# Kernel optimization log

Hardware: AMD Instinct MI355X
Metric: run time of the kernel (lower is better)

## Reference

```python
import jax, jax.numpy as jnp
import numpy as np
import math

B, T, N, E = 16, 12, 2000, 8000
D, GAT_HEADS, NHEAD, FF, L, HORIZON = 64, 4, 4, 128, 2, 3
M = B * N  # batched node count


def setup_inputs() -> dict:
    key = jax.random.key(0)
    ks = jax.random.split(key, 16)

    def nrm(k, shape, s=0.1):
        return jax.random.normal(k, shape, jnp.float32) * s

    return dict(
        x_seq=jax.random.normal(ks[0], (B, T, N), jnp.float32),
        edge_index=jax.random.randint(ks[1], (2, E), 0, N),
        # GATConv 1: in_dim=1 -> 4 heads x 8 = 32
        W1=nrm(ks[2], (1, 32)),
        att_src1=nrm(ks[3], (GAT_HEADS, 8)),
        att_dst1=nrm(ks[4], (GAT_HEADS, 8)),
        b1=jnp.zeros((32,), jnp.float32),
        # GATConv 2: 32 -> 4 heads x 16 = 64
        W2=nrm(ks[5], (32, 64)),
        att_src2=nrm(ks[6], (GAT_HEADS, 16)),
        att_dst2=nrm(ks[7], (GAT_HEADS, 16)),
        b2=jnp.zeros((64,), jnp.float32),
        # TransformerEncoder (post-LN, relu), stacked over L layers
        Wqkv=nrm(ks[8], (L, 3 * D, D)), bqkv=jnp.zeros((L, 3 * D), jnp.float32),
        Wo=nrm(ks[9], (L, D, D)), bo=jnp.zeros((L, D), jnp.float32),
        Wf1=nrm(ks[10], (L, FF, D)), bf1=jnp.zeros((L, FF), jnp.float32),
        Wf2=nrm(ks[11], (L, D, FF)), bf2=jnp.zeros((L, D), jnp.float32),
        g1=jnp.ones((L, D), jnp.float32), be1=jnp.zeros((L, D), jnp.float32),
        g2=jnp.ones((L, D), jnp.float32), be2=jnp.zeros((L, D), jnp.float32),
        # prediction head
        Wh=nrm(ks[12], (HORIZON, D)), bh=jnp.zeros((HORIZON,), jnp.float32),
    )


def _layer_norm(x, g, b, eps=1e-5):
    mu = x.mean(-1, keepdims=True)
    var = ((x - mu) ** 2).mean(-1, keepdims=True)
    return (x - mu) * jax.lax.rsqrt(var + eps) * g + b


def _gat(x, src, dst, W, a_src, a_dst, bias, H, C, num_nodes):
    # PyG GATConv (concat=True, eval mode). x: [M, in] -> [M, H*C]
    h = (x @ W).reshape(-1, H, C)                                  # [M,H,C]
    e = jax.nn.leaky_relu((h * a_src).sum(-1)[src] + (h * a_dst).sum(-1)[dst], 0.2)  # [Etot,H]
    m = jax.ops.segment_max(e, dst, num_segments=num_nodes)
    w = jnp.exp(e - m[dst])
    s = jax.ops.segment_sum(w, dst, num_segments=num_nodes)
    alpha = w / (s[dst] + 1e-16)
    out = jax.ops.segment_sum(h[src] * alpha[:, :, None], dst, num_segments=num_nodes)
    return out.reshape(-1, H * C) + bias


def _forward(x_seq, edge_index, W1, att_src1, att_dst1, b1, W2, att_src2, att_dst2, b2,
             Wqkv, bqkv, Wo, bo, Wf1, bf1, Wf2, bf2, g1, be1, g2, be2, Wh, bh):
    # batch edge index with per-graph node offsets, then add self loops (PyG default)
    offs = (jnp.arange(B) * N)[:, None]
    loops = jnp.arange(M)
    src = jnp.concatenate([(edge_index[0][None] + offs).reshape(-1), loops])
    dst = jnp.concatenate([(edge_index[1][None] + offs).reshape(-1), loops])

    xt = x_seq.transpose(1, 0, 2).reshape(T, M, 1)  # per-timestep node features

    def gnn_step(x):
        h = jax.nn.relu(_gat(x, src, dst, W1, att_src1, att_dst1, b1, GAT_HEADS, 8, M))
        return jax.nn.relu(_gat(h, src, dst, W2, att_src2, att_dst2, b2, GAT_HEADS, 16, M))

    seq = jax.vmap(gnn_step)(xt)  # [T, M, D]

    # sinusoidal positional encoding over time axis
    pos = jnp.arange(T, dtype=jnp.float32)[:, None]
    div = jnp.exp(jnp.arange(0, D, 2, dtype=jnp.float32) * (-math.log(10000.0) / D))
    pe = jnp.zeros((T, D), jnp.float32)
    pe = pe.at[:, 0::2].set(jnp.sin(pos * div)).at[:, 1::2].set(jnp.cos(pos * div))
    seq = seq + pe[:, None, :]

    hd = D // NHEAD
    scale = 1.0 / math.sqrt(hd)
    for i in range(L):  # post-LN transformer encoder layers
        qkv = seq @ Wqkv[i].T + bqkv[i]
        q, k, v = jnp.split(qkv, 3, axis=-1)
        q = q.reshape(T, M, NHEAD, hd)
        k = k.reshape(T, M, NHEAD, hd)
        v = v.reshape(T, M, NHEAD, hd)
        sc = jnp.einsum('tmhd,smhd->mhts', q, k) * scale  # [M,H,T,T]
        attn = jax.nn.softmax(sc, axis=-1)
        o = jnp.einsum('mhts,smhd->tmhd', attn, v).reshape(T, M, D)
        seq = _layer_norm(seq + (o @ Wo[i].T + bo[i]), g1[i], be1[i])
        ff = jax.nn.relu(seq @ Wf1[i].T + bf1[i]) @ Wf2[i].T + bf2[i]
        seq = _layer_norm(seq + ff, g2[i], be2[i])

    final = seq[-1]  # [M, D]
    return (final @ Wh.T + bh).reshape(B, N, HORIZON).transpose(0, 2, 1)  # [B, horizon, N]


def reference(x_seq, edge_index, W1, att_src1, att_dst1, b1, W2, att_src2, att_dst2, b2,
              Wqkv, bqkv, Wo, bo, Wf1, bf1, Wf2, bf2, g1, be1, g2, be2, Wh, bh):
    return _forward(x_seq, edge_index, W1, att_src1, att_dst1, b1, W2, att_src2, att_dst2, b2,
                    Wqkv, bqkv, Wo, bo, Wf1, bf1, Wf2, bf2, g1, be1, g2, be2, Wh, bh)
```

## Files before the change

### kernel.cpp

```cpp
#include <hip/hip_runtime.h>
#include <hip/hip_bf16.h>

#define B_ 16
#define T_ 12
#define N_ 2000
#define E_ 8000
#define M_ 32000
#define ETOT (B_*E_ + M_)
#define D_ 64

typedef __hip_bfloat16 bf16;
typedef unsigned short u16;
typedef __attribute__((ext_vector_type(8))) _Float16 half8;
typedef __attribute__((ext_vector_type(2))) _Float16 h2v;
typedef __attribute__((ext_vector_type(4))) float f32x4;

__device__ __forceinline__ float bfu(u16 u){ return __uint_as_float(((unsigned int)u)<<16); }
__device__ __forceinline__ u16 f2bu(float f){
  unsigned int x = __float_as_uint(f);
  x += 0x7FFFu + ((x >> 16) & 1u);
  return (u16)(x >> 16);
}
__device__ __forceinline__ u16 f2h(float f){
  _Float16 h = (_Float16)f; u16 r; __builtin_memcpy(&r, &h, 2); return r;
}
__device__ __forceinline__ float h2f(u16 u){
  _Float16 h; __builtin_memcpy(&h, &u, 2); return (float)h;
}
__device__ __forceinline__ h2v u2h(unsigned u){ h2v r; __builtin_memcpy(&r,&u,4); return r; }

__global__ void k_prep(const float* __restrict__ Wqkv, const float* __restrict__ Wo,
                       const float* __restrict__ Wf1, const float* __restrict__ Wf2,
                       u16* __restrict__ wqB, u16* __restrict__ woB,
                       u16* __restrict__ w1B, u16* __restrict__ w2B,
                       float* __restrict__ peT){
  int i = blockIdx.x*256 + threadIdx.x;
  if(i < 24576){
    int l=i/12288, r=i-l*12288;
    int nt=r>>10, r2=r&1023, c=r2>>9, r3=r2&511, lane=r3>>3, jj=r3&7;
    int m=lane&15, q=lane>>4;
    wqB[i] = f2h(Wqkv[l*12288 + (nt*16+m)*64 + c*32 + q*8 + jj]);
  } else if(i < 32768){
    int k2=i-24576;
    int l=k2>>12, r=k2&4095;
    int nt=r>>10, r2=r&1023, c=r2>>9, r3=r2&511, lane=r3>>3, jj=r3&7;
    int m=lane&15, q=lane>>4;
    woB[k2] = f2h(Wo[l*4096 + (nt*16+m)*64 + c*32 + q*8 + jj]);
  } else if(i < 49152){
    int k2=i-32768;
    int l=k2>>13, r=k2&8191;
    int nt=r>>10, r2=r&1023, c=r2>>9, r3=r2&511, lane=r3>>3, jj=r3&7;
    int m=lane&15, q=lane>>4;
    w1B[k2] = f2h(Wf1[l*8192 + (nt*16+m)*64 + c*32 + q*8 + jj]);
  } else if(i < 65536){
    int k2=i-49152;
    int l=k2>>13, r=k2&8191;
    int nt=r>>11, r2=r&2047, c=r2>>9, r3=r2&511, lane=r3>>3, jj=r3&7;
    int m=lane&15, q=lane>>4;
    w2B[k2] = f2h(Wf2[l*8192 + (nt*16+m)*128 + c*32 + q*8 + jj]);
  } else {
    int i2 = i - 65536;
    if(i2 < 768){
      int t=i2>>6, ch=i2&63;
      float ang = (float)t * __expf(-0.14391156463f * (float)(ch & ~1));
      peT[i2] = (ch&1) ? __cosf(ang) : __sinf(ang);
    }
  }
}

__global__ void k_zero(int* __restrict__ p, int n){
  int i = blockIdx.x*256 + threadIdx.x; if(i<n) p[i]=0;
}

__global__ void k_hist(const int* __restrict__ ei, int* __restrict__ deg){
  int e = blockIdx.x*256 + threadIdx.x; if(e>=ETOT) return;
  int dst;
  if (e < B_*E_){ int b = e / E_; int k = e - b*E_; dst = ei[E_ + k] + b*N_; }
  else dst = e - B_*E_;
  atomicAdd(&deg[dst], 1);
}

__global__ void k_scan1(const int* __restrict__ deg, int* __restrict__ offs, int* __restrict__ bsums){
  __shared__ int s[256];
  int tid = threadIdx.x; int g = blockIdx.x*256 + tid;
  s[tid] = deg[g]; __syncthreads();
  for(int off=1; off<256; off<<=1){
    int a = (tid>=off) ? s[tid-off] : 0; __syncthreads();
    s[tid] += a; __syncthreads();
  }
  offs[g+1] = s[tid];
  if(tid==255) bsums[blockIdx.x] = s[255];
}

__global__ void k_scan2(const int* __restrict__ bsums, int* __restrict__ boffs){
  __shared__ int s[128];
  int tid = threadIdx.x;
  int v = (tid<125) ? bsums[tid] : 0;
  s[tid] = v; __syncthreads();
  for(int off=1; off<128; off<<=1){
    int a = (tid>=off) ? s[tid-off] : 0; __syncthreads();
    s[tid] += a; __syncthreads();
  }
  if(tid<125) boffs[tid] = s[tid] - v;
}

__global__ void k_scan3(int* __restrict__ offs, const int* __restrict__ boffs){
  int tid = threadIdx.x; int g = blockIdx.x*256 + tid;
  offs[g+1] += boffs[blockIdx.x];
  if(g==0) offs[0]=0;
}

__global__ void k_scatter(const int* __restrict__ ei, const int* __restrict__ offs,
                          int* __restrict__ cursor, int* __restrict__ csr){
  int e = blockIdx.x*256 + threadIdx.x; if(e>=ETOT) return;
  int src, dst;
  if (e < B_*E_){ int b=e/E_; int k=e-b*E_; src=ei[k]+b*N_; dst=ei[E_+k]+b*N_; }
  else { src = e - B_*E_; dst = src; }
  int pos = atomicAdd(&cursor[dst], 1);
  csr[offs[dst]+pos] = src;
}

__global__ __launch_bounds__(256) void k_gat12(
  const float* __restrict__ x_seq, const float* __restrict__ W1,
  const float* __restrict__ as1, const float* __restrict__ ad1, const float* __restrict__ b1,
  const float* __restrict__ W2, const float* __restrict__ as2, const float* __restrict__ ad2,
  const int* __restrict__ offs, const int* __restrict__ csr,
  u16* __restrict__ h2u, float* __restrict__ asc, float* __restrict__ adc)
{
  __shared__ float W2s[2048];
  __shared__ float a2s[64], a2d[64];
  int tid = threadIdx.x;
  for(int i=tid;i<2048;i+=256) W2s[i]=W2[i];
  if(tid<64){ a2s[tid]=as2[tid]; a2d[tid]=ad2[tid]; }
  __syncthreads();

  int t = blockIdx.y;
  int id = blockIdx.x*256 + tid;
  int m = id>>2, l4 = id&3;

  float sS[4], sD[4];
  #pragma unroll
  for(int h=0;h<4;h++){
    float a=0.f, d=0.f;
    #pragma unroll
    for(int c=0;c<8;c++){ float w=W1[h*8+c]; a+=w*as1[h*8+c]; d+=w*ad1[h*8+c]; }
    sS[h]=a; sD[h]=d;
  }
  unsigned um=(unsigned)m, b=um/N_, n=um-b*N_;
  const float* xsl = x_seq + (size_t)(b*T_+t)*N_;
  float xm = xsl[n];
  int e0=offs[m], e1=offs[m+1];
  float sum[4]={0,0,0,0}, ax[4]={0,0,0,0};
  for(int e=e0+l4; e<e1; e+=4){
    unsigned s=(unsigned)csr[e]; unsigned sn=s - (s/N_)*N_;
    float xv = xsl[sn];
    #pragma unroll
    for(int h=0;h<4;h++){
      float ee = xv*sS[h] + xm*sD[h]; ee = ee>0.f ? ee : 0.2f*ee;
      float w = __expf(ee); sum[h]+=w; ax[h]+=w*xv;
    }
  }
  float A[4];
  #pragma unroll
  for(int h=0;h<4;h++){
    sum[h] += __shfl_xor(sum[h],1); sum[h] += __shfl_xor(sum[h],2);
    ax[h]  += __shfl_xor(ax[h],1);  ax[h]  += __shfl_xor(ax[h],2);
    A[h] = ax[h]/(sum[h]+1e-16f);
  }

  float acc[16];
  #pragma unroll
  for(int c=0;c<16;c++) acc[c]=0.f;
  #pragma unroll
  for(int k=0;k<32;k++){
    int hs = k>>3;
    float v = A[hs]*W1[k] + b1[k]; v = v>0.f ? v : 0.f;
    #pragma unroll
    for(int c=0;c<16;c++) acc[c] += v*W2s[k*64 + l4*16 + c];
  }
  uint2* hp = (uint2*)(h2u + ((size_t)t*M_ + m)*64 + l4*16);
  #pragma unroll
  for(int c2=0;c2<4;c2++){
    uint2 p;
    p.x = (unsigned)f2bu(acc[4*c2+0]) | ((unsigned)f2bu(acc[4*c2+1])<<16);
    p.y = (unsigned)f2bu(acc[4*c2+2]) | ((unsigned)f2bu(acc[4*c2+3])<<16);
    hp[c2] = p;
  }
  float ss=0.f, sd=0.f;
  #pragma unroll
  for(int c=0;c<16;c++){ ss += acc[c]*a2s[l4*16+c]; sd += acc[c]*a2d[l4*16+c]; }
  asc[((size_t)t*M_+m)*4+l4]=ss; adc[((size_t)t*M_+m)*4+l4]=sd;
}

__global__ __launch_bounds__(256) void k_gat2b(
  const u16* __restrict__ h2u, const float* __restrict__ asc, const float* __restrict__ adc,
  const float* __restrict__ b2, const int* __restrict__ offs, const int* __restrict__ csr,
  const float* __restrict__ peT, u16* __restrict__ seq)
{
  int t = blockIdx.y;
  int id = blockIdx.x*256 + threadIdx.x;
  int m = id>>2, h = id&3;
  float am = adc[((size_t)t*M_+m)*4+h];
  int e0=offs[m], e1=offs[m+1];
  float sum=0.f;
  float A[16];
  #pragma unroll
  for(int c=0;c<16;c++) A[c]=0.f;
  for(int e=e0;e<e1;e++){
    int s=csr[e];
    float ee = asc[((size_t)t*M_+s)*4+h] + am; ee = ee>0.f ? ee : 0.2f*ee;
    float w = __expf(ee); sum += w;
    const uint2* hp = (const uint2*)(h2u + ((size_t)t*M_ + s)*64 + h*16);
    #pragma unroll
    for(int c2=0;c2<4;c2++){
      uint2 p = hp[c2];
      A[4*c2+0] += w*bfu((u16)(p.x));
      A[4*c2+1] += w*bfu((u16)(p.x>>16));
      A[4*c2+2] += w*bfu((u16)(p.y));
      A[4*c2+3] += w*bfu((u16)(p.y>>16));
    }
  }
  float inv = 1.f/(sum + 1e-16f);
  #pragma unroll
  for(int c=0;c<16;c++){
    int ch = h*16 + c;
    float v = A[c]*inv + b2[ch]; v = v>0.f ? v : 0.f;
    seq[((size_t)t*M_ + m)*64 + ch] = f2h(v + peT[t*64+ch]);
  }
}

__global__ __launch_bounds__(192) void k_layer2(
  u16* __restrict__ seq,
  const u16* __restrict__ wqB, const u16* __restrict__ woB,
  const u16* __restrict__ w1B, const u16* __restrict__ w2B,
  const float* __restrict__ bqkv, const float* __restrict__ bo,
  const float* __restrict__ bf1,  const float* __restrict__ bf2,
  const float* __restrict__ g1,   const float* __restrict__ be1,
  const float* __restrict__ g2,   const float* __restrict__ be2)
{
  __shared__ __align__(16) u16 X[3456];
  __shared__ __align__(16) u16 QKV[10368];
  u16* Hd = QKV + 3456;
  int tid=threadIdx.x, w=tid>>6, lane=tid&63;
  int m=lane&15, q=lane>>4;
  int r = w*16 + m;

  int trr[4]; size_t base_rr[4];
  #pragma unroll
  for(int rg=0;rg<4;rg++){
    int rc = w*16 + q*4 + rg;
    int nn = rc/12; trr[rg] = rc - nn*12;
    base_rr[rg] = ((size_t)trr[rg]*M_ + (size_t)blockIdx.x*4 + nn)*64;
  }

  #pragma unroll
  for(int rr=0; rr<16; rr++){
    int row = w*16+rr;
    int nn = row/12, tt = row-nn*12;
    X[row*72+lane] = seq[((size_t)tt*M_ + (size_t)blockIdx.x*4+nn)*64 + lane];
  }

  #pragma unroll 1
  for(int l=0; l<2; l++){
    const half8* wqv = (const half8*)(wqB + l*24576/2*0 + (size_t)l*12288);
    const half8* wov = (const half8*)(woB + (size_t)l*4096);
    const half8* w1v = (const half8*)(w1B + (size_t)l*8192);
    const half8* w2v = (const half8*)(w2B + (size_t)l*8192);
    const float* bq = bqkv + l*192;
    const float* boL = bo + l*64;
    const float* b1L = bf1 + l*128;
    const float* b2L = bf2 + l*64;
    const float* g1L = g1 + l*64, *be1L = be1 + l*64;
    const float* g2L = g2 + l*64, *be2L = be2 + l*64;

    half8 xa0 = *(const half8*)&X[r*72 + q*8];
    half8 xa1 = *(const half8*)&X[r*72 + 32 + q*8];
    #pragma unroll
    for(int nt=0; nt<12; nt++){
      f32x4 acc={0.f,0.f,0.f,0.f};
      acc = __builtin_amdgcn_mfma_f32_16x16x32_f16(xa0, wqv[(nt*2+0)*64+lane], acc,0,0,0);
      acc = __builtin_amdgcn_mfma_f32_16x16x32_f16(xa1, wqv[(nt*2+1)*64+lane], acc,0,0,0);
      int cg = nt*16+m; float bias = bq[cg];
      int s = nt>>2, lc = cg&63;
      #pragma unroll
      for(int rg=0;rg<4;rg++){
        int row = w*16 + q*4 + rg;
        QKV[s*3456 + row*72 + lc] = f2h(acc[rg]+bias);
      }
    }
    __syncthreads();

    {
      int an = tid/48, rem = tid - an*48;
      int ah = rem/12, at = rem - ah*12;
      u16* qrow = &QKV[(an*12+at)*72 + ah*16];
      uint4 qa = ((const uint4*)qrow)[0], qb = ((const uint4*)qrow)[1];
      float s[12];
      #pragma unroll
      for(int t2=0;t2<12;t2++){
        const uint4* kp = (const uint4*)&QKV[3456 + (an*12+t2)*72 + ah*16];
        uint4 ka=kp[0], kb=kp[1];
        float d=0.f;
        d=__builtin_amdgcn_fdot2(u2h(qa.x),u2h(ka.x),d,false);
        d=__builtin_amdgcn_fdot2(u2h(qa.y),u2h(ka.y),d,false);
        d=__builtin_amdgcn_fdot2(u2h(qa.z),u2h(ka.z),d,false);
        d=__builtin_amdgcn_fdot2(u2h(qa.w),u2h(ka.w),d,false);
        d=__builtin_amdgcn_fdot2(u2h(qb.x),u2h(kb.x),d,false);
        d=__builtin_amdgcn_fdot2(u2h(qb.y),u2h(kb.y),d,false);
        d=__builtin_amdgcn_fdot2(u2h(qb.z),u2h(kb.z),d,false);
        d=__builtin_amdgcn_fdot2(u2h(qb.w),u2h(kb.w),d,false);
        s[t2] = d*0.25f;
      }
      float mx=s[0];
      #pragma unroll
      for(int t2=1;t2<12;t2++) mx=fmaxf(mx,s[t2]);
      float sum=0.f;
      #pragma unroll
      for(int t2=0;t2<12;t2++){ s[t2]=__expf(s[t2]-mx); sum+=s[t2]; }
      float inv=1.f/sum;
      half8 o0, o1;
      #pragma unroll
      for(int i=0;i<8;i++){ o0[i]=(_Float16)0.f; o1[i]=(_Float16)0.f; }
      #pragma unroll
      for(int t2=0;t2<12;t2++){
        const half8* vr = (const half8*)&QKV[6912 + (an*12+t2)*72 + ah*16];
        _Float16 wh = (_Float16)s[t2];
        o0 += vr[0]*wh; o1 += vr[1]*wh;
      }
      _Float16 ih = (_Float16)inv;
      ((half8*)qrow)[0]=o0*ih; ((half8*)qrow)[1]=o1*ih;
    }
    __syncthreads();

    half8 oa0 = *(const half8*)&QKV[r*72 + q*8];
    half8 oa1 = *(const half8*)&QKV[r*72 + 32 + q*8];
    float y[4][4];
    #pragma unroll
    for(int nt=0;nt<4;nt++){
      f32x4 acc={0.f,0.f,0.f,0.f};
      acc = __builtin_amdgcn_mfma_f32_16x16x32_f16(oa0, wov[(nt*2+0)*64+lane], acc,0,0,0);
      acc = __builtin_amdgcn_mfma_f32_16x16x32_f16(oa1, wov[(nt*2+1)*64+lane], acc,0,0,0);
      int col=nt*16+m; float bias=boL[col];
      #pragma unroll
      for(int rg=0;rg<4;rg++)
        y[nt][rg] = acc[rg] + bias + h2f(X[(w*16+q*4+rg)*72 + col]);
    }
    float mu[4], rs[4];
    #pragma unroll
    for(int rg=0;rg<4;rg++){
      float sm=(y[0][rg]+y[1][rg])+(y[2][rg]+y[3][rg]);
      sm+=__shfl_xor(sm,1); sm+=__shfl_xor(sm,2); sm+=__shfl_xor(sm,4); sm+=__shfl_xor(sm,8);
      mu[rg]=sm*(1.f/64.f);
      float d0=y[0][rg]-mu[rg],d1=y[1][rg]-mu[rg],d2=y[2][rg]-mu[rg],d3=y[3][rg]-mu[rg];
      float vv=(d0*d0+d1*d1)+(d2*d2+d3*d3);
      vv+=__shfl_xor(vv,1); vv+=__shfl_xor(vv,2); vv+=__shfl_xor(vv,4); vv+=__shfl_xor(vv,8);
      rs[rg]=rsqrtf(vv*(1.f/64.f)+1e-5f);
    }
    #pragma unroll
    for(int nt=0;nt<4;nt++){
      int col=nt*16+m; float g=g1L[col], be=be1L[col];
      #pragma unroll
      for(int rg=0;rg<4;rg++){
        float v=(y[nt][rg]-mu[rg])*rs[rg]*g+be;
        y[nt][rg]=v;
        QKV[(w*16+q*4+rg)*72 + col]=f2h(v);
      }
    }

    half8 ya0 = *(const half8*)&QKV[r*72 + q*8];
    half8 ya1 = *(const half8*)&QKV[r*72 + 32 + q*8];
    #pragma unroll
    for(int nt=0;nt<8;nt++){
      f32x4 acc={0.f,0.f,0.f,0.f};
      acc = __builtin_amdgcn_mfma_f32_16x16x32_f16(ya0, w1v[(nt*2+0)*64+lane], acc,0,0,0);
      acc = __builtin_amdgcn_mfma_f32_16x16x32_f16(ya1, w1v[(nt*2+1)*64+lane], acc,0,0,0);
      float bias=b1L[nt*16+m];
      #pragma unroll
      for(int rg=0;rg<4;rg++)
        Hd[(w*16+q*4+rg)*136 + nt*16+m] = f2h(fmaxf(acc[rg]+bias, 0.f));
    }

    half8 ha[4];
    #pragma unroll
    for(int c=0;c<4;c++)
      ha[c] = *(const half8*)&Hd[r*136 + c*32 + q*8];
    #pragma unroll
    for(int nt=0;nt<4;nt++){
      f32x4 acc={0.f,0.f,0.f,0.f};
      #pragma unroll
      for(int c=0;c<4;c++)
        acc = __builtin_amdgcn_mfma_f32_16x16x32_f16(ha[c], w2v[(nt*4+c)*64+lane], acc,0,0,0);
      int col=nt*16+m; float bias=b2L[col];
      #pragma unroll
      for(int rg=0;rg<4;rg++)
        y[nt][rg] = acc[rg] + bias + y[nt][rg];
    }
    #pragma unroll
    for(int rg=0;rg<4;rg++){
      float sm=(y[0][rg]+y[1][rg])+(y[2][rg]+y[3][rg]);
      sm+=__shfl_xor(sm,1); sm+=__shfl_xor(sm,2); sm+=__shfl_xor(sm,4); sm+=__shfl_xor(sm,8);
      mu[rg]=sm*(1.f/64.f);
      float d0=y[0][rg]-mu[rg],d1=y[1][rg]-mu[rg],d2=y[2][rg]-mu[rg],d3=y[3][rg]-mu[rg];
      float vv=(d0*d0+d1*d1)+(d2*d2+d3*d3);
      vv+=__shfl_xor(vv,1); vv+=__shfl_xor(vv,2); vv+=__shfl_xor(vv,4); vv+=__shfl_xor(vv,8);
      rs[rg]=rsqrtf(vv*(1.f/64.f)+1e-5f);
    }
    if(l==0){
      #pragma unroll
      for(int nt=0;nt<4;nt++){
        int col=nt*16+m; float g=g2L[col], be=be2L[col];
        #pragma unroll
        for(int rg=0;rg<4;rg++)
          X[(w*16+q*4+rg)*72 + col] = f2h((y[nt][rg]-mu[rg])*rs[rg]*g + be);
      }
      __syncthreads();
    } else {
      #pragma unroll
      for(int nt=0;nt<4;nt++){
        int col=nt*16+m; float g=g2L[col], be=be2L[col];
        #pragma unroll
        for(int rg=0;rg<4;rg++){
          if(trr[rg]==11)
            seq[base_rr[rg] + col] = f2h((y[nt][rg]-mu[rg])*rs[rg]*g + be);
        }
      }
    }
  }
}

__global__ void k_head(const u16* __restrict__ seq, const float* __restrict__ Wh,
                       const float* __restrict__ bh, float* __restrict__ out){
  int m = blockIdx.x*256 + threadIdx.x; if(m>=M_) return;
  const u16* row = seq + ((size_t)11*M_ + m)*64;
  float a0=bh[0], a1=bh[1], a2=bh[2];
  #pragma unroll
  for(int d=0;d<64;d++){
    float x = h2f(row[d]);
    a0 += x*Wh[d]; a1 += x*Wh[64+d]; a2 += x*Wh[128+d];
  }
  unsigned b=(unsigned)m/N_, n=(unsigned)m-b*N_;
  out[(b*3+0)*N_+n] = a0;
  out[(b*3+1)*N_+n] = a1;
  out[(b*3+2)*N_+n] = a2;
}

extern "C" void kernel_launch(void* const* d_in, const int* in_sizes, int n_in,
                              void* d_out, int out_size, void* d_ws, size_t ws_size,
                              hipStream_t stream)
{
  const float* x_seq=(const float*)d_in[0];
  const int*   ei   =(const int*)d_in[1];
  const float* W1   =(const float*)d_in[2];
  const float* as1  =(const float*)d_in[3];
  const float* ad1  =(const float*)d_in[4];
  const float* b1   =(const float*)d_in[5];
  const float* W2   =(const float*)d_in[6];
  const float* as2  =(const float*)d_in[7];
  const float* ad2  =(const float*)d_in[8];
  const float* b2   =(const float*)d_in[9];
  const float* Wqkv =(const float*)d_in[10];
  const float* bqkv =(const float*)d_in[11];
  const float* Wo   =(const float*)d_in[12];
  const float* bo   =(const float*)d_in[13];
  const float* Wf1  =(const float*)d_in[14];
  const float* bf1p =(const float*)d_in[15];
  const float* Wf2  =(const float*)d_in[16];
  const float* bf2p =(const float*)d_in[17];
  const float* g1   =(const float*)d_in[18];
  const float* be1  =(const float*)d_in[19];
  const float* g2   =(const float*)d_in[20];
  const float* be2  =(const float*)d_in[21];
  const float* Wh   =(const float*)d_in[22];
  const float* bh   =(const float*)d_in[23];

  u16* seqh   = (u16*)d_ws;
  float* asc  = (float*)(seqh + 24576000);
  float* adc  = asc + 1536000;
  int* deg    = (int*)(adc + 1536000);
  int* cursor = deg + M_;
  int* offs   = cursor + M_;
  int* bsums  = offs + (M_ + 2);
  int* boffs  = bsums + 128;
  int* csr    = boffs + 128;
  u16* h2u    = (u16*)(csr + ETOT);
  u16* wqB    = h2u + (size_t)T_*M_*64;
  u16* woB    = wqB + 24576;
  u16* w1B    = woB + 8192;
  u16* w2B    = w1B + 16384;
  float* peT  = (float*)(w2B + 16384);

  k_prep   <<<dim3(260), dim3(256), 0, stream>>>(Wqkv, Wo, Wf1, Wf2, wqB, woB, w1B, w2B, peT);

  k_zero   <<<dim3((2*M_+255)/256), dim3(256), 0, stream>>>(deg, 2*M_);
  k_hist   <<<dim3((ETOT+255)/256), dim3(256), 0, stream>>>(ei, deg);
  k_scan1  <<<dim3(125), dim3(256), 0, stream>>>(deg, offs, bsums);
  k_scan2  <<<dim3(1),   dim3(128), 0, stream>>>(bsums, boffs);
  k_scan3  <<<dim3(125), dim3(256), 0, stream>>>(offs, boffs);
  k_scatter<<<dim3((ETOT+255)/256), dim3(256), 0, stream>>>(ei, offs, cursor, csr);

  k_gat12<<<dim3(500,T_), dim3(256), 0, stream>>>(x_seq, W1, as1, ad1, b1,
                                                  W2, as2, ad2, offs, csr, h2u, asc, adc);
  k_gat2b<<<dim3(500,T_), dim3(256), 0, stream>>>(h2u, asc, adc, b2, offs, csr, peT, seqh);

  k_layer2<<<dim3(8000), dim3(192), 0, stream>>>(seqh,
      wqB, woB, w1B, w2B,
      bqkv, bo, bf1p, bf2p,
      g1, be1, g2, be2);

  k_head<<<dim3(125), dim3(256), 0, stream>>>(seqh, Wh, bh, (float*)d_out);
}
```

Before: 415.0 us.

## Transpose MFMA operands in transformer layer, vectorize LDS stores, store local CSR indices

```diff
diff --git a/kernel.cpp b/kernel.cpp
--- a/kernel.cpp
+++ b/kernel.cpp
@@ -28,6 +28,9 @@
   _Float16 h; __builtin_memcpy(&h, &u, 2); return (float)h;
 }
 __device__ __forceinline__ h2v u2h(unsigned u){ h2v r; __builtin_memcpy(&r,&u,4); return r; }
+__device__ __forceinline__ unsigned pk2(float a, float b){
+  return (unsigned)f2h(a) | ((unsigned)f2h(b)<<16);
+}
 
 __global__ void k_prep(const float* __restrict__ Wqkv, const float* __restrict__ Wo,
                        const float* __restrict__ Wf1, const float* __restrict__ Wf2,
@@ -68,10 +71,6 @@
   }
 }
 
-__global__ void k_zero(int* __restrict__ p, int n){
-  int i = blockIdx.x*256 + threadIdx.x; if(i<n) p[i]=0;
-}
-
 __global__ void k_hist(const int* __restrict__ ei, int* __restrict__ deg){
   int e = blockIdx.x*256 + threadIdx.x; if(e>=ETOT) return;
   int dst;
@@ -113,11 +112,11 @@
 __global__ void k_scatter(const int* __restrict__ ei, const int* __restrict__ offs,
                           int* __restrict__ cursor, int* __restrict__ csr){
   int e = blockIdx.x*256 + threadIdx.x; if(e>=ETOT) return;
-  int src, dst;
-  if (e < B_*E_){ int b=e/E_; int k=e-b*E_; src=ei[k]+b*N_; dst=ei[E_+k]+b*N_; }
-  else { src = e - B_*E_; dst = src; }
+  int srcl, dst;
+  if (e < B_*E_){ int b=e/E_; int k=e-b*E_; srcl=ei[k]; dst=ei[E_+k]+b*N_; }
+  else { dst = e - B_*E_; int b=dst/N_; srcl = dst - b*N_; }
   int pos = atomicAdd(&cursor[dst], 1);
-  csr[offs[dst]+pos] = src;
+  csr[offs[dst]+pos] = srcl;
 }
 
 __global__ __launch_bounds__(256) void k_gat12(
@@ -152,8 +151,7 @@
   int e0=offs[m], e1=offs[m+1];
   float sum[4]={0,0,0,0}, ax[4]={0,0,0,0};
   for(int e=e0+l4; e<e1; e+=4){
-    unsigned s=(unsigned)csr[e]; unsigned sn=s - (s/N_)*N_;
-    float xv = xsl[sn];
+    float xv = xsl[csr[e]];
     #pragma unroll
     for(int h=0;h<4;h++){
       float ee = xv*sS[h] + xm*sD[h]; ee = ee>0.f ? ee : 0.2f*ee;
@@ -200,6 +198,8 @@
   int t = blockIdx.y;
   int id = blockIdx.x*256 + threadIdx.x;
   int m = id>>2, h = id&3;
+  unsigned um=(unsigned)m, b=um/N_;
+  size_t base_s = (size_t)t*M_ + (size_t)b*N_;
   float am = adc[((size_t)t*M_+m)*4+h];
   int e0=offs[m], e1=offs[m+1];
   float sum=0.f;
@@ -207,10 +207,10 @@
   #pragma unroll
   for(int c=0;c<16;c++) A[c]=0.f;
   for(int e=e0;e<e1;e++){
-    int s=csr[e];
-    float ee = asc[((size_t)t*M_+s)*4+h] + am; ee = ee>0.f ? ee : 0.2f*ee;
+    size_t s = base_s + (unsigned)csr[e];
+    float ee = asc[s*4+h] + am; ee = ee>0.f ? ee : 0.2f*ee;
     float w = __expf(ee); sum += w;
-    const uint2* hp = (const uint2*)(h2u + ((size_t)t*M_ + s)*64 + h*16);
+    const uint2* hp = (const uint2*)(h2u + s*64 + h*16);
     #pragma unroll
     for(int c2=0;c2<4;c2++){
       uint2 p = hp[c2];
@@ -244,14 +244,9 @@
   int tid=threadIdx.x, w=tid>>6, lane=tid&63;
   int m=lane&15, q=lane>>4;
   int r = w*16 + m;
-
-  int trr[4]; size_t base_rr[4];
-  #pragma unroll
-  for(int rg=0;rg<4;rg++){
-    int rc = w*16 + q*4 + rg;
-    int nn = rc/12; trr[rg] = rc - nn*12;
-    base_rr[rg] = ((size_t)trr[rg]*M_ + (size_t)blockIdx.x*4 + nn)*64;
-  }
+  int nr = r/12, tr = r - nr*12;
+  int node_r = blockIdx.x*4 + nr;
+  size_t xoff = ((size_t)tr*M_ + node_r)*64;
 
   #pragma unroll
   for(int rr=0; rr<16; rr++){
@@ -262,7 +257,7 @@
 
   #pragma unroll 1
   for(int l=0; l<2; l++){
-    const half8* wqv = (const half8*)(wqB + l*24576/2*0 + (size_t)l*12288);
+    const half8* wqv = (const half8*)(wqB + (size_t)l*12288);
     const half8* wov = (const half8*)(woB + (size_t)l*4096);
     const half8* w1v = (const half8*)(w1B + (size_t)l*8192);
     const half8* w2v = (const half8*)(w2B + (size_t)l*8192);
@@ -273,20 +268,20 @@
     const float* g1L = g1 + l*64, *be1L = be1 + l*64;
     const float* g2L = g2 + l*64, *be2L = be2 + l*64;
 
-    half8 xa0 = *(const half8*)&X[r*72 + q*8];
-    half8 xa1 = *(const half8*)&X[r*72 + 32 + q*8];
+    half8 xb0 = *(const half8*)&X[r*72 + q*8];
+    half8 xb1 = *(const half8*)&X[r*72 + 32 + q*8];
     #pragma unroll
     for(int nt=0; nt<12; nt++){
       f32x4 acc={0.f,0.f,0.f,0.f};
-      acc = __builtin_amdgcn_mfma_f32_16x16x32_f16(xa0, wqv[(nt*2+0)*64+lane], acc,0,0,0);
-      acc = __builtin_amdgcn_mfma_f32_16x16x32_f16(xa1, wqv[(nt*2+1)*64+lane], acc,0,0,0);
-      int cg = nt*16+m; float bias = bq[cg];
-      int s = nt>>2, lc = cg&63;
-      #pragma unroll
-      for(int rg=0;rg<4;rg++){
-        int row = w*16 + q*4 + rg;
-        QKV[s*3456 + row*72 + lc] = f2h(acc[rg]+bias);
-      }
+      acc = __builtin_amdgcn_mfma_f32_16x16x32_f16(wqv[(nt*2+0)*64+lane], xb0, acc,0,0,0);
+      acc = __builtin_amdgcn_mfma_f32_16x16x32_f16(wqv[(nt*2+1)*64+lane], xb1, acc,0,0,0);
+      int cg0 = nt*16 + q*4;
+      float4 bv = *(const float4*)&bq[cg0];
+      int s = cg0>>6, lc = cg0&63;
+      uint2 pk;
+      pk.x = pk2(acc[0]+bv.x, acc[1]+bv.y);
+      pk.y = pk2(acc[2]+bv.z, acc[3]+bv.w);
+      *(uint2*)&QKV[s*3456 + r*72 + lc] = pk;
     }
     __syncthreads();
 
@@ -332,96 +327,117 @@
     }
     __syncthreads();
 
-    half8 oa0 = *(const half8*)&QKV[r*72 + q*8];
-    half8 oa1 = *(const half8*)&QKV[r*72 + 32 + q*8];
+    half8 ob0 = *(const half8*)&QKV[r*72 + q*8];
+    half8 ob1 = *(const half8*)&QKV[r*72 + 32 + q*8];
     float y[4][4];
     #pragma unroll
     for(int nt=0;nt<4;nt++){
       f32x4 acc={0.f,0.f,0.f,0.f};
-      acc = __builtin_amdgcn_mfma_f32_16x16x32_f16(oa0, wov[(nt*2+0)*64+lane], acc,0,0,0);
-      acc = __builtin_amdgcn_mfma_f32_16x16x32_f16(oa1, wov[(nt*2+1)*64+lane], acc,0,0,0);
-      int col=nt*16+m; float bias=boL[col];
-      #pragma unroll
-      for(int rg=0;rg<4;rg++)
-        y[nt][rg] = acc[rg] + bias + h2f(X[(w*16+q*4+rg)*72 + col]);
-    }
-    float mu[4], rs[4];
-    #pragma unroll
-    for(int rg=0;rg<4;rg++){
-      float sm=(y[0][rg]+y[1][rg])+(y[2][rg]+y[3][rg]);
-      sm+=__shfl_xor(sm,1); sm+=__shfl_xor(sm,2); sm+=__shfl_xor(sm,4); sm+=__shfl_xor(sm,8);
-      mu[rg]=sm*(1.f/64.f);
-      float d0=y[0][rg]-mu[rg],d1=y[1][rg]-mu[rg],d2=y[2][rg]-mu[rg],d3=y[3][rg]-mu[rg];
-      float vv=(d0*d0+d1*d1)+(d2*d2+d3*d3);
-      vv+=__shfl_xor(vv,1); vv+=__shfl_xor(vv,2); vv+=__shfl_xor(vv,4); vv+=__shfl_xor(vv,8);
-      rs[rg]=rsqrtf(vv*(1.f/64.f)+1e-5f);
-    }
+      acc = __builtin_amdgcn_mfma_f32_16x16x32_f16(wov[(nt*2+0)*64+lane], ob0, acc,0,0,0);
+      acc = __builtin_amdgcn_mfma_f32_16x16x32_f16(wov[(nt*2+1)*64+lane], ob1, acc,0,0,0);
+      int ch0=nt*16+q*4;
+      float4 bv = *(const float4*)&boL[ch0];
+      uint2 xr_ = *(const uint2*)&X[r*72 + ch0];
+      h2v x0=u2h(xr_.x), x1=u2h(xr_.y);
+      y[nt][0] = acc[0] + bv.x + (float)x0[0];
+      y[nt][1] = acc[1] + bv.y + (float)x0[1];
+      y[nt][2] = acc[2] + bv.z + (float)x1[0];
+      y[nt][3] = acc[3] + bv.w + (float)x1[1];
+    }
+    float sm=0.f;
+    #pragma unroll
+    for(int nt=0;nt<4;nt++) sm += (y[nt][0]+y[nt][1])+(y[nt][2]+y[nt][3]);
+    sm += __shfl_xor(sm,16); sm += __shfl_xor(sm,32);
+    float mu = sm*(1.f/64.f);
+    float vv=0.f;
     #pragma unroll
     for(int nt=0;nt<4;nt++){
-      int col=nt*16+m; float g=g1L[col], be=be1L[col];
-      #pragma unroll
-      for(int rg=0;rg<4;rg++){
-        float v=(y[nt][rg]-mu[rg])*rs[rg]*g+be;
-        y[nt][rg]=v;
-        QKV[(w*16+q*4+rg)*72 + col]=f2h(v);
-      }
-    }
-
-    half8 ya0 = *(const half8*)&QKV[r*72 + q*8];
-    half8 ya1 = *(const half8*)&QKV[r*72 + 32 + q*8];
+      float d0=y[nt][0]-mu, d1=y[nt][1]-mu, d2=y[nt][2]-mu, d3=y[nt][3]-mu;
+      vv += (d0*d0+d1*d1)+(d2*d2+d3*d3);
+    }
+    vv += __shfl_xor(vv,16); vv += __shfl_xor(vv,32);
+    float rs = rsqrtf(vv*(1.f/64.f)+1e-5f);
+    #pragma unroll
+    for(int nt=0;nt<4;nt++){
+      int ch0=nt*16+q*4;
+      float4 gv = *(const float4*)&g1L[ch0];
+      float4 bev= *(const float4*)&be1L[ch0];
+      y[nt][0]=(y[nt][0]-mu)*rs*gv.x+bev.x;
+      y[nt][1]=(y[nt][1]-mu)*rs*gv.y+bev.y;
+      y[nt][2]=(y[nt][2]-mu)*rs*gv.z+bev.z;
+      y[nt][3]=(y[nt][3]-mu)*rs*gv.w+bev.w;
+      uint2 pk; pk.x=pk2(y[nt][0],y[nt][1]); pk.y=pk2(y[nt][2],y[nt][3]);
+      *(uint2*)&QKV[r*72 + ch0] = pk;
+    }
+
+    half8 yb0 = *(const half8*)&QKV[r*72 + q*8];
+    half8 yb1 = *(const half8*)&QKV[r*72 + 32 + q*8];
     #pragma unroll
     for(int nt=0;nt<8;nt++){
       f32x4 acc={0.f,0.f,0.f,0.f};
-      acc = __builtin_amdgcn_mfma_f32_16x16x32_f16(ya0, w1v[(nt*2+0)*64+lane], acc,0,0,0);
-      acc = __builtin_amdgcn_mfma_f32_16x16x32_f16(ya1, w1v[(nt*2+1)*64+lane], acc,0,0,0);
-      float bias=b1L[nt*16+m];
-      #pragma unroll
-      for(int rg=0;rg<4;rg++)
-        Hd[(w*16+q*4+rg)*136 + nt*16+m] = f2h(fmaxf(acc[rg]+bias, 0.f));
-    }
-
-    half8 ha[4];
+      acc = __builtin_amdgcn_mfma_f32_16x16x32_f16(w1v[(nt*2+0)*64+lane], yb0, acc,0,0,0);
+      acc = __builtin_amdgcn_mfma_f32_16x16x32_f16(w1v[(nt*2+1)*64+lane], yb1, acc,0,0,0);
+      int hc0=nt*16+q*4;
+      float4 bv = *(const float4*)&b1L[hc0];
+      uint2 pk;
+      pk.x = pk2(fmaxf(acc[0]+bv.x,0.f), fmaxf(acc[1]+bv.y,0.f));
+      pk.y = pk2(fmaxf(acc[2]+bv.z,0.f), fmaxf(acc[3]+bv.w,0.f));
+      *(uint2*)&Hd[r*136 + hc0] = pk;
+    }
+
+    half8 hb[4];
     #pragma unroll
     for(int c=0;c<4;c++)
-      ha[c] = *(const half8*)&Hd[r*136 + c*32 + q*8];
+      hb[c] = *(const half8*)&Hd[r*136 + c*32 + q*8];
     #pragma unroll
     for(int nt=0;nt<4;nt++){
       f32x4 acc={0.f,0.f,0.f,0.f};
       #pragma unroll
       for(int c=0;c<4;c++)
-        acc = __builtin_amdgcn_mfma_f32_16x16x32_f16(ha[c], w2v[(nt*4+c)*64+lane], acc,0,0,0);
-      int col=nt*16+m; float bias=b2L[col];
-      #pragma unroll
-      for(int rg=0;rg<4;rg++)
-        y[nt][rg] = acc[rg] + bias + y[nt][rg];
-    }
-    #pragma unroll
-    for(int rg=0;rg<4;rg++){
-      float sm=(y[0][rg]+y[1][rg])+(y[2][rg]+y[3][rg]);
-      sm+=__shfl_xor(sm,1); sm+=__shfl_xor(sm,2); sm+=__shfl_xor(sm,4); sm+=__shfl_xor(sm,8);
-      mu[rg]=sm*(1.f/64.f);
-      float d0=y[0][rg]-mu[rg],d1=y[1][rg]-mu[rg],d2=y[2][rg]-mu[rg],d3=y[3][rg]-mu[rg];
-      float vv=(d0*d0+d1*d1)+(d2*d2+d3*d3);
-      vv+=__shfl_xor(vv,1); vv+=__shfl_xor(vv,2); vv+=__shfl_xor(vv,4); vv+=__shfl_xor(vv,8);
-      rs[rg]=rsqrtf(vv*(1.f/64.f)+1e-5f);
-    }
+        acc = __builtin_amdgcn_mfma_f32_16x16x32_f16(w2v[(nt*4+c)*64+lane], hb[c], acc,0,0,0);
+      int ch0=nt*16+q*4;
+      float4 bv = *(const float4*)&b2L[ch0];
+      y[nt][0] = acc[0] + bv.x + y[nt][0];
+      y[nt][1] = acc[1] + bv.y + y[nt][1];
+      y[nt][2] = acc[2] + bv.z + y[nt][2];
+      y[nt][3] = acc[3] + bv.w + y[nt][3];
+    }
+    sm=0.f;
+    #pragma unroll
+    for(int nt=0;nt<4;nt++) sm += (y[nt][0]+y[nt][1])+(y[nt][2]+y[nt][3]);
+    sm += __shfl_xor(sm,16); sm += __shfl_xor(sm,32);
+    mu = sm*(1.f/64.f);
+    vv=0.f;
+    #pragma unroll
+    for(int nt=0;nt<4;nt++){
+      float d0=y[nt][0]-mu, d1=y[nt][1]-mu, d2=y[nt][2]-mu, d3=y[nt][3]-mu;
+      vv += (d0*d0+d1*d1)+(d2*d2+d3*d3);
+    }
+    vv += __shfl_xor(vv,16); vv += __shfl_xor(vv,32);
+    rs = rsqrtf(vv*(1.f/64.f)+1e-5f);
     if(l==0){
       #pragma unroll
       for(int nt=0;nt<4;nt++){
-        int col=nt*16+m; float g=g2L[col], be=be2L[col];
-        #pragma unroll
-        for(int rg=0;rg<4;rg++)
-          X[(w*16+q*4+rg)*72 + col] = f2h((y[nt][rg]-mu[rg])*rs[rg]*g + be);
+        int ch0=nt*16+q*4;
+        float4 gv = *(const float4*)&g2L[ch0];
+        float4 bev= *(const float4*)&be2L[ch0];
+        uint2 pk;
+        pk.x = pk2((y[nt][0]-mu)*rs*gv.x+bev.x, (y[nt][1]-mu)*rs*gv.y+bev.y);
+        pk.y = pk2((y[nt][2]-mu)*rs*gv.z+bev.z, (y[nt][3]-mu)*rs*gv.w+bev.w);
+        *(uint2*)&X[r*72 + ch0] = pk;
       }
       __syncthreads();
     } else {
-      #pragma unroll
-      for(int nt=0;nt<4;nt++){
-        int col=nt*16+m; float g=g2L[col], be=be2L[col];
+      if(tr==11){
         #pragma unroll
-        for(int rg=0;rg<4;rg++){
-          if(trr[rg]==11)
-            seq[base_rr[rg] + col] = f2h((y[nt][rg]-mu[rg])*rs[rg]*g + be);
+        for(int nt=0;nt<4;nt++){
+          int ch0=nt*16+q*4;
+          float4 gv = *(const float4*)&g2L[ch0];
+          float4 bev= *(const float4*)&be2L[ch0];
+          uint2 pk;
+          pk.x = pk2((y[nt][0]-mu)*rs*gv.x+bev.x, (y[nt][1]-mu)*rs*gv.y+bev.y);
+          pk.y = pk2((y[nt][2]-mu)*rs*gv.z+bev.z, (y[nt][3]-mu)*rs*gv.w+bev.w);
+          *(uint2*)&seq[xoff + ch0] = pk;
         }
       }
     }
@@ -491,7 +507,7 @@
 
   k_prep   <<<dim3(260), dim3(256), 0, stream>>>(Wqkv, Wo, Wf1, Wf2, wqB, woB, w1B, w2B, peT);
 
-  k_zero   <<<dim3((2*M_+255)/256), dim3(256), 0, stream>>>(deg, 2*M_);
+  hipMemsetAsync(deg, 0, (size_t)2*M_*sizeof(int), stream);
   k_hist   <<<dim3((ETOT+255)/256), dim3(256), 0, stream>>>(ei, deg);
   k_scan1  <<<dim3(125), dim3(256), 0, stream>>>(deg, offs, bsums);
   k_scan2  <<<dim3(1),   dim3(128), 0, stream>>>(bsums, boffs);
```

Measured after the change: 420.4 us. About the same (+1.3%).
